# Kernel tuning notes

Measured on AMD Instinct MI355X. Metric: run time of the kernel, lower is better.

Reference implementation:

```python
import jax, jax.numpy as jnp
import numpy as np

B, L, D = 2, 2048, 2048
H, Hd = 16, 128


def _rotary_cos_sin(max_len, dim, base=10000.0):
    inv_freq = 1.0 / (base ** (np.arange(0, dim, 2, dtype=np.float32) / dim))
    t = np.arange(max_len, dtype=np.float32)
    freqs = np.outer(t, inv_freq)                      # [L, dim/2]
    emb = np.concatenate([freqs, freqs], axis=-1)      # [L, dim]
    cos = np.cos(emb)[None, None]                      # [1,1,L,dim]
    sin = np.sin(emb)[None, None]
    return jnp.asarray(cos), jnp.asarray(sin)


def setup_inputs() -> dict:
    key = jax.random.key(0)
    ks = jax.random.split(key, 5)
    hidden_states = jax.random.normal(ks[0], (B, L, D), dtype=jnp.float32)
    cos, sin = _rotary_cos_sin(L, Hd)
    s = 1.0 / np.sqrt(D)
    wq = jax.random.normal(ks[1], (H * Hd, D), dtype=jnp.float32) * s
    wk = jax.random.normal(ks[2], (H * Hd, D), dtype=jnp.float32) * s
    wv = jax.random.normal(ks[3], (H * Hd, D), dtype=jnp.float32) * s
    wo = jax.random.normal(ks[4], (D, H * Hd), dtype=jnp.float32) * s
    return {"hidden_states": hidden_states, "cos": cos, "sin": sin,
            "wq": wq, "wk": wk, "wv": wv, "wo": wo}


def _rotate_half(x):
    x1, x2 = jnp.split(x, 2, axis=-1)
    return jnp.concatenate([-x2, x1], axis=-1)


def reference(hidden_states, cos, sin, wq, wk, wv, wo):
    b, l, d = hidden_states.shape
    # QKV projections -> [B, H, L, Hd]
    q = (hidden_states @ wq.T).reshape(b, l, H, Hd).transpose(0, 2, 1, 3)
    k = (hidden_states @ wk.T).reshape(b, l, H, Hd).transpose(0, 2, 1, 3)
    v = (hidden_states @ wv.T).reshape(b, l, H, Hd).transpose(0, 2, 1, 3)
    c = cos[:, :, :l, :]
    s = sin[:, :, :l, :]
    q = q * c + _rotate_half(q) * s
    k = k * c + _rotate_half(k) * s
    # SDPA (non-causal, default scale = 1/sqrt(head_dim))
    scale = 1.0 / jnp.sqrt(jnp.asarray(Hd, dtype=q.dtype))
    scores = jnp.einsum('bhqd,bhkd->bhqk', q, k) * scale
    attn = jax.nn.softmax(scores, axis=-1)
    out = jnp.einsum('bhqk,bhkd->bhqd', attn, v)       # [B,H,L,Hd]
    out = out.transpose(0, 2, 1, 3).reshape(b, l, H * Hd)
    return out @ wo.T
```

## Files before the change

kernel.cpp:

```cpp
#include <hip/hip_runtime.h>

constexpr int Bb = 2;
constexpr int Ll = 2048;
constexpr int Dd = 2048;
constexpr int Hh = 16;
constexpr int Hd = 128;
constexpr int M  = Bb * Ll;

typedef __attribute__((ext_vector_type(8)))  short s16x8;
typedef __attribute__((ext_vector_type(4)))  float f32x4;
typedef __attribute__((ext_vector_type(16))) float f32x16;

__device__ __forceinline__ unsigned short f2bf(float f) {
    union { float f; unsigned u; } v; v.f = f;
    unsigned r = v.u + 0x7fffu + ((v.u >> 16) & 1u);
    return (unsigned short)(r >> 16);
}
__device__ __forceinline__ float bf2f(unsigned short b) {
    union { unsigned u; float f; } v; v.u = ((unsigned)b) << 16;
    return v.f;
}
__device__ __forceinline__ float fast_exp2(float x) {
#if __has_builtin(__builtin_amdgcn_exp2f)
    return __builtin_amdgcn_exp2f(x);
#else
    return exp2f(x);
#endif
}

__device__ __forceinline__ void gld16(const void* g, void* l) {
#if __has_builtin(__builtin_amdgcn_global_load_lds)
    __builtin_amdgcn_global_load_lds(
        (const __attribute__((address_space(1))) unsigned int*)g,
        (__attribute__((address_space(3))) unsigned int*)l, 16, 0, 0);
#else
    int lane = threadIdx.x & 63;
    ((int4*)l)[lane] = ((const int4*)g)[0];
#endif
}

__global__ __launch_bounds__(256)
void f2bf_all(const float* __restrict__ x,  const float* __restrict__ wq,
              const float* __restrict__ wk, const float* __restrict__ wv,
              const float* __restrict__ wo,
              unsigned short* __restrict__ Xb,  unsigned short* __restrict__ Wqb,
              unsigned short* __restrict__ Wkb, unsigned short* __restrict__ Wvb,
              unsigned short* __restrict__ Wob)
{
    int bid = blockIdx.x;
    const float* in; unsigned short* out; int off;
    if      (bid <  8192) { in = x;  out = Xb;  off = bid; }
    else if (bid < 12288) { in = wq; out = Wqb; off = bid - 8192; }
    else if (bid < 16384) { in = wk; out = Wkb; off = bid - 12288; }
    else if (bid < 20480) { in = wv; out = Wvb; off = bid - 16384; }
    else                  { in = wo; out = Wob; off = bid - 20480; }
    int i = (off * 256 + threadIdx.x) * 4;
    float4 v = *(const float4*)(in + i);
    ushort4 o;
    o.x = f2bf(v.x); o.y = f2bf(v.y); o.z = f2bf(v.z); o.w = f2bf(v.w);
    *(ushort4*)(out + i) = o;
}

__global__ __launch_bounds__(256, 2)
void mfma_gemm_qkv(const unsigned short* __restrict__ A,
                   const unsigned short* __restrict__ Wall,
                   unsigned short* __restrict__ Oq,
                   unsigned short* __restrict__ Ok,
                   unsigned short* __restrict__ Ov)
{
    constexpr int K  = 2048;
    constexpr int NT = K / 64;
    constexpr int BM = 128, BN = 192;
    constexpr int SLOT_US = (BM + BN) * 64;

    __shared__ unsigned short lds[2 * SLOT_US];

    const int t    = threadIdx.x;
    const int w    = t >> 6, lane = t & 63;
    const int wm   = w >> 1, wn = w & 1;
    const int m0   = blockIdx.y * BM, n0 = blockIdx.x * BN;
    const int r16  = lane & 15, q4 = lane >> 4;
    const int lxor = (r16 & 7) << 4;

    const int srow8 = lane >> 3;
    const int sgcol = (((lane & 7) ^ srow8) << 4);
    const char* Agb = (const char*)A;
    const char* Wgb = (const char*)Wall;

    f32x4 acc[4][6];
#pragma unroll
    for (int i = 0; i < 4; ++i)
#pragma unroll
        for (int j = 0; j < 6; ++j)
            acc[i][j] = (f32x4){0.f, 0.f, 0.f, 0.f};

#define STAGE_ALL(tt, sl) do {                                               \
    _Pragma("unroll") for (int p = 0; p < 4; ++p) {                          \
        int ia_ = w * 4 + p;                                                 \
        gld16(Agb + (size_t)(m0 + ia_ * 8 + srow8) * (K * 2) + (tt) * 128 + sgcol, \
              &lds[(sl) * SLOT_US + ia_ * 512]);                             \
    }                                                                        \
    _Pragma("unroll") for (int p = 0; p < 6; ++p) {                          \
        int ib_ = w * 6 + p;                                                 \
        gld16(Wgb + (size_t)(n0 + ib_ * 8 + srow8) * (K * 2) + (tt) * 128 + sgcol, \
              &lds[(sl) * SLOT_US + BM * 64 + ib_ * 512]);                   \
    }                                                                        \
} while (0)

#define MFMA24() do {                                                        \
    __builtin_amdgcn_s_setprio(1);                                           \
    _Pragma("unroll") for (int mi = 0; mi < 4; ++mi)                         \
    _Pragma("unroll") for (int ni = 0; ni < 6; ++ni)                         \
        acc[mi][ni] = __builtin_amdgcn_mfma_f32_16x16x32_bf16(                \
            a[mi], b[ni], acc[mi][ni], 0, 0, 0);                             \
    __builtin_amdgcn_s_setprio(0);                                           \
} while (0)

    STAGE_ALL(0, 0);
    asm volatile("s_waitcnt vmcnt(0)" ::: "memory");
    __builtin_amdgcn_s_barrier();
    asm volatile("" ::: "memory");

    for (int tt = 0; tt < NT; ++tt) {
        const int slot = tt & 1;
        const char* Ab = (const char*)&lds[slot * SLOT_US];
        const char* Bp = (const char*)&lds[slot * SLOT_US + BM * 64];
        const int c0 = (q4 * 16) ^ lxor;
        const int c1 = (64 + q4 * 16) ^ lxor;

        s16x8 a[4], b[6];

#pragma unroll
        for (int mi = 0; mi < 4; ++mi)
            a[mi] = *(const s16x8*)(Ab + (wm * 64 + mi * 16 + r16) * 128 + c0);
#pragma unroll
        for (int ni = 0; ni < 6; ++ni)
            b[ni] = *(const s16x8*)(Bp + (wn * 96 + ni * 16 + r16) * 128 + c0);
        if (tt + 1 < NT) STAGE_ALL(tt + 1, slot ^ 1);
        MFMA24();

#pragma unroll
        for (int mi = 0; mi < 4; ++mi)
            a[mi] = *(const s16x8*)(Ab + (wm * 64 + mi * 16 + r16) * 128 + c1);
#pragma unroll
        for (int ni = 0; ni < 6; ++ni)
            b[ni] = *(const s16x8*)(Bp + (wn * 96 + ni * 16 + r16) * 128 + c1);
        MFMA24();

        asm volatile("s_waitcnt vmcnt(0)" ::: "memory");
        __builtin_amdgcn_s_barrier();
        asm volatile("" ::: "memory");
    }
#undef STAGE_ALL
#undef MFMA24

#pragma unroll
    for (int ni = 0; ni < 6; ++ni) {
        int nb   = n0 + wn * 96 + ni * 16;
        int nsel = nb >> 11;
        int nr   = nb & 2047;
        int h    = nr >> 7;
        int d    = (nr & 127) + r16;
        if (nsel < 2) {
            unsigned short* O = nsel ? Ok : Oq;
#pragma unroll
            for (int mi = 0; mi < 4; ++mi)
#pragma unroll
                for (int r = 0; r < 4; ++r) {
                    int m = m0 + wm * 64 + mi * 16 + q4 * 4 + r;
                    int b = m >> 11, l = m & 2047;
                    O[(((size_t)b * Hh + h) * Ll + l) * Hd + d] =
                        f2bf(acc[mi][ni][r]);
                }
        } else {
#pragma unroll
            for (int mi = 0; mi < 4; ++mi) {
                int mb = m0 + wm * 64 + mi * 16 + q4 * 4;
                int b = mb >> 11, l = mb & 2047;
                ushort4 pk;
                pk.x = f2bf(acc[mi][ni][0]);
                pk.y = f2bf(acc[mi][ni][1]);
                pk.z = f2bf(acc[mi][ni][2]);
                pk.w = f2bf(acc[mi][ni][3]);
                *(ushort4*)&Ov[(((size_t)b * Hh + h) * Hd + d) * Ll + l] = pk;
            }
        }
    }
}

__global__ __launch_bounds__(256, 2)
void mfma_gemm_out(const unsigned short* __restrict__ A,
                   const unsigned short* __restrict__ W,
                   float* __restrict__ FO)
{
    constexpr int K  = 2048;
    constexpr int NT = K / 64;
    constexpr int BM = 128, BN = 128;
    constexpr int SLOT_US = (BM + BN) * 64;

    __shared__ unsigned short lds[2 * SLOT_US];

    const int t    = threadIdx.x;
    const int w    = t >> 6, lane = t & 63;
    const int wm   = w >> 1, wn = w & 1;
    const int m0   = blockIdx.y * BM, n0 = blockIdx.x * BN;
    const int r16  = lane & 15, q4 = lane >> 4;
    const int lxor = (r16 & 7) << 4;

    const int srow8 = lane >> 3;
    const int sgcol = (((lane & 7) ^ srow8) << 4);
    const char* Agb = (const char*)A;
    const char* Wgb = (const char*)W;

    f32x4 acc[4][4];
#pragma unroll
    for (int i = 0; i < 4; ++i)
#pragma unroll
        for (int j = 0; j < 4; ++j)
            acc[i][j] = (f32x4){0.f, 0.f, 0.f, 0.f};

#define STAGE_ALL(tt, sl) do {                                               \
    _Pragma("unroll") for (int p = 0; p < 4; ++p) {                          \
        int ia_ = w * 4 + p;                                                 \
        gld16(Agb + (size_t)(m0 + ia_ * 8 + srow8) * (K * 2) + (tt) * 128 + sgcol, \
              &lds[(sl) * SLOT_US + ia_ * 512]);                             \
    }                                                                        \
    _Pragma("unroll") for (int p = 0; p < 4; ++p) {                          \
        int ib_ = w * 4 + p;                                                 \
        gld16(Wgb + (size_t)(n0 + ib_ * 8 + srow8) * (K * 2) + (tt) * 128 + sgcol, \
              &lds[(sl) * SLOT_US + BM * 64 + ib_ * 512]);                   \
    }                                                                        \
} while (0)

#define MFMA16() do {                                                        \
    __builtin_amdgcn_s_setprio(1);                                           \
    _Pragma("unroll") for (int mi = 0; mi < 4; ++mi)                         \
    _Pragma("unroll") for (int ni = 0; ni < 4; ++ni)                         \
        acc[mi][ni] = __builtin_amdgcn_mfma_f32_16x16x32_bf16(                \
            a[mi], b[ni], acc[mi][ni], 0, 0, 0);                             \
    __builtin_amdgcn_s_setprio(0);                                           \
} while (0)

    STAGE_ALL(0, 0);
    asm volatile("s_waitcnt vmcnt(0)" ::: "memory");
    __builtin_amdgcn_s_barrier();
    asm volatile("" ::: "memory");

    for (int tt = 0; tt < NT; ++tt) {
        const int slot = tt & 1;
        const char* Ab = (const char*)&lds[slot * SLOT_US];
        const char* Bp = (const char*)&lds[slot * SLOT_US + BM * 64];
        const int c0 = (q4 * 16) ^ lxor;
        const int c1 = (64 + q4 * 16) ^ lxor;

        s16x8 a[4], b[4];

#pragma unroll
        for (int mi = 0; mi < 4; ++mi)
            a[mi] = *(const s16x8*)(Ab + (wm * 64 + mi * 16 + r16) * 128 + c0);
#pragma unroll
        for (int ni = 0; ni < 4; ++ni)
            b[ni] = *(const s16x8*)(Bp + (wn * 64 + ni * 16 + r16) * 128 + c0);
        if (tt + 1 < NT) STAGE_ALL(tt + 1, slot ^ 1);
        MFMA16();

#pragma unroll
        for (int mi = 0; mi < 4; ++mi)
            a[mi] = *(const s16x8*)(Ab + (wm * 64 + mi * 16 + r16) * 128 + c1);
#pragma unroll
        for (int ni = 0; ni < 4; ++ni)
            b[ni] = *(const s16x8*)(Bp + (wn * 64 + ni * 16 + r16) * 128 + c1);
        MFMA16();

        asm volatile("s_waitcnt vmcnt(0)" ::: "memory");
        __builtin_amdgcn_s_barrier();
        asm volatile("" ::: "memory");
    }
#undef STAGE_ALL
#undef MFMA16

#pragma unroll
    for (int mi = 0; mi < 4; ++mi)
#pragma unroll
        for (int ni = 0; ni < 4; ++ni) {
            int n = n0 + wn * 64 + ni * 16 + r16;
#pragma unroll
            for (int r = 0; r < 4; ++r) {
                int m = m0 + wm * 64 + mi * 16 + q4 * 4 + r;
                FO[(size_t)m * Dd + n] = acc[mi][ni][r];
            }
        }
}

__global__ __launch_bounds__(256)
void rope_bf16(unsigned short* __restrict__ q, unsigned short* __restrict__ k,
               const float* __restrict__ cosb, const float* __restrict__ sinb)
{
    const float QS = 0.1275175f;
    const int t = threadIdx.x;
    int rblk = blockIdx.x;
    unsigned short* base;
    float sc;
    if (rblk < 4096) { base = q; sc = QS; }
    else             { base = k; sc = 1.0f; rblk -= 4096; }

    const int row = rblk * 16 + (t >> 4);
    const int l   = row & (Ll - 1);
    const int d0  = (t & 15) * 8;
    unsigned short* xr = base + (size_t)row * Hd;

    s16x8 v0 = *(const s16x8*)(xr + d0);
    s16x8 vp = *(const s16x8*)(xr + (d0 ^ 64));
    const float* cp = cosb + (size_t)l * Hd + d0;
    const float* sp = sinb + (size_t)l * Hd + d0;
    float4 c0 = *(const float4*)cp,       c1 = *(const float4*)(cp + 4);
    float4 sa = *(const float4*)sp,       sb = *(const float4*)(sp + 4);
    const float cc[8] = {c0.x, c0.y, c0.z, c0.w, c1.x, c1.y, c1.z, c1.w};
    const float ss[8] = {sa.x, sa.y, sa.z, sa.w, sb.x, sb.y, sb.z, sb.w};
    const float sgn = (d0 < 64) ? -1.f : 1.f;

    s16x8 o;
#pragma unroll
    for (int j = 0; j < 8; ++j) {
        float a = bf2f((unsigned short)v0[j]);
        float p = bf2f((unsigned short)vp[j]);
        float res = fmaf(a, cc[j], sgn * p * ss[j]) * sc;
        o[j] = (short)f2bf(res);
    }
    asm volatile("" ::: "memory");
    *(s16x8*)(xr + d0) = o;
}

__global__ __launch_bounds__(256)
void flash_attn(const unsigned short* __restrict__ q,
                const unsigned short* __restrict__ k,
                const unsigned short* __restrict__ vT,
                unsigned short* __restrict__ ctx)
{
    __shared__ unsigned short Ks[2][64 * 128];
    __shared__ unsigned short Vs[2][128 * 64];
    __shared__ unsigned short Ps[4][32 * 64];

    const int t = threadIdx.x;
    const int w = t >> 6, lane = t & 63;
    const int n32 = lane & 31, half = lane >> 5;
    const int bh = blockIdx.x >> 4;
    const int l0 = (blockIdx.x & 15) * 128;

    const unsigned short* qb = q  + ((size_t)bh * Ll + l0 + w * 32) * Hd;
    const unsigned short* kb = k  + (size_t)bh * Ll * Hd;
    const unsigned short* vb = vT + (size_t)bh * Hd * Ll;

    const int k_r = lane >> 4, k_u = lane & 15;
    const int v_r = lane >> 3, v_u = lane & 7;

#define STAGE(J0, bsel) do {                                                  \
    _Pragma("unroll") for (int p = 0; p < 4; ++p) {                           \
        int j_ = w * 4 + p;                                                   \
        int row_ = j_ * 4 + k_r;                                              \
        gld16(kb + (size_t)((J0) + row_) * Hd + ((k_u ^ (row_ & 7)) * 8),     \
              &Ks[bsel][j_ * 512]);                                           \
    }                                                                         \
    _Pragma("unroll") for (int p = 0; p < 4; ++p) {                           \
        int j_ = w * 4 + p;                                                   \
        int row_ = j_ * 8 + v_r;                                              \
        gld16(vb + (size_t)row_ * Ll + (J0) + ((v_u ^ (row_ & 7)) * 8),       \
              &Vs[bsel][j_ * 512]);                                           \
    }                                                                         \
} while (0)

    s16x8 qf[8];
#pragma unroll
    for (int ks = 0; ks < 8; ++ks)
        qf[ks] = *(const s16x8*)(qb + (size_t)n32 * Hd + ks * 16 + half * 8);

    f32x16 o[4];
    float lacc[16];
#pragma unroll
    for (int nt = 0; nt < 4; ++nt)
#pragma unroll
        for (int r = 0; r < 16; ++r) o[nt][r] = 0.f;
#pragma unroll
    for (int r = 0; r < 16; ++r) lacc[r] = 0.f;

    unsigned short* Pw = Ps[w];
    const int psw = (n32 & 7) << 3;

    STAGE(0, 0);
    __syncthreads();

    int buf = 0;
    for (int j0 = 0; j0 < Ll; j0 += 64) {
        if (j0 + 64 < Ll) STAGE(j0 + 64, buf ^ 1);

        f32x16 s0, s1;
#pragma unroll
        for (int r = 0; r < 16; ++r) { s0[r] = 0.f; s1[r] = 0.f; }
        __builtin_amdgcn_s_setprio(1);
#pragma unroll
        for (int ks = 0; ks < 8; ++ks) {
            int kc = (ks * 16 + half * 8) ^ psw;
            s16x8 b0 = *(const s16x8*)&Ks[buf][n32 * 128 + kc];
            s16x8 b1 = *(const s16x8*)&Ks[buf][(32 + n32) * 128 + kc];
            s0 = __builtin_amdgcn_mfma_f32_32x32x16_bf16(qf[ks], b0, s0, 0, 0, 0);
            s1 = __builtin_amdgcn_mfma_f32_32x32x16_bf16(qf[ks], b1, s1, 0, 0, 0);
        }
        __builtin_amdgcn_s_setprio(0);

#pragma unroll
        for (int r = 0; r < 16; ++r) {
            int mrow = (r & 3) + 8 * (r >> 2) + 4 * half;
            int sw = (mrow & 7) << 3;
            float p0 = fast_exp2(s0[r]);
            float p1 = fast_exp2(s1[r]);
            lacc[r] += p0 + p1;
            union { float f; unsigned u; } u0, u1;
            u0.f = p0; u1.f = p1;
            Pw[mrow * 64 + (n32 ^ sw)]        = (unsigned short)((u0.u + 0x8000u) >> 16);
            Pw[mrow * 64 + ((32 + n32) ^ sw)] = (unsigned short)((u1.u + 0x8000u) >> 16);
        }

        __builtin_amdgcn_s_setprio(1);
#pragma unroll
        for (int kst = 0; kst < 4; ++kst) {
            int cc = (kst * 16 + half * 8) ^ psw;
            s16x8 pf2 = *(const s16x8*)&Pw[n32 * 64 + cc];
#pragma unroll
            for (int nt = 0; nt < 4; ++nt) {
                s16x8 vf = *(const s16x8*)&Vs[buf][(nt * 32 + n32) * 64 + cc];
                o[nt] = __builtin_amdgcn_mfma_f32_32x32x16_bf16(pf2, vf, o[nt], 0, 0, 0);
            }
        }
        __builtin_amdgcn_s_setprio(0);

        __syncthreads();
        buf ^= 1;
    }
#undef STAGE

    float linv[16];
#pragma unroll
    for (int r = 0; r < 16; ++r) {
        float s = lacc[r];
        s += __shfl_xor(s, 1, 64);
        s += __shfl_xor(s, 2, 64);
        s += __shfl_xor(s, 4, 64);
        s += __shfl_xor(s, 8, 64);
        s += __shfl_xor(s, 16, 64);
        linv[r] = 1.0f / s;
    }

    const int b = bh >> 4, h = bh & 15;
#pragma unroll
    for (int nt = 0; nt < 4; ++nt)
#pragma unroll
        for (int r = 0; r < 16; ++r) {
            int mrow = (r & 3) + 8 * (r >> 2) + 4 * half;
            int lq = l0 + w * 32 + mrow;
            ctx[((size_t)(b * Ll + lq)) * Dd + h * Hd + nt * 32 + n32] =
                f2bf(o[nt][r] * linv[r]);
        }
}

extern "C" void kernel_launch(void* const* d_in, const int* in_sizes, int n_in,
                              void* d_out, int out_size, void* d_ws, size_t ws_size,
                              hipStream_t stream)
{
    const float* hs   = (const float*)d_in[0];
    const float* cosb = (const float*)d_in[1];
    const float* sinb = (const float*)d_in[2];
    const float* wq   = (const float*)d_in[3];
    const float* wk   = (const float*)d_in[4];
    const float* wv   = (const float*)d_in[5];
    const float* wo   = (const float*)d_in[6];
    float* out = (float*)d_out;

    char* ws = (char*)d_ws;
    unsigned short* Xb  = (unsigned short*)(ws);
    unsigned short* Wqb = (unsigned short*)(ws + (16ull << 20));
    unsigned short* Wkb = (unsigned short*)(ws + (24ull << 20));
    unsigned short* Wvb = (unsigned short*)(ws + (32ull << 20));
    unsigned short* Wob = (unsigned short*)(ws + (40ull << 20));
    unsigned short* qb  = (unsigned short*)(ws + (48ull << 20));
    unsigned short* kb  = (unsigned short*)(ws + (64ull << 20));
    unsigned short* vTb = (unsigned short*)(ws + (80ull << 20));
    unsigned short* ctx = Xb;

    f2bf_all<<<dim3(24576), dim3(256), 0, stream>>>(
        hs, wq, wk, wv, wo, Xb, Wqb, Wkb, Wvb, Wob);

    mfma_gemm_qkv<<<dim3(6144 / 192, M / 128), dim3(256), 0, stream>>>(
        Xb, Wqb, qb, kb, vTb);

    rope_bf16<<<dim3(2 * (Bb * Hh * Ll) / 16), dim3(256), 0, stream>>>(
        qb, kb, cosb, sinb);

    flash_attn<<<dim3(Bb * Hh * (Ll / 128)), dim3(256), 0, stream>>>(qb, kb, vTb, ctx);

    mfma_gemm_out<<<dim3(Dd / 128, M / 128), dim3(256), 0, stream>>>(
        ctx, Wob, out);
}
```

Measured before the change: 379.6 us.

## Fuse RoPE and Q scaling into QKV GEMM epilogue via LDS staging

Removes the separate rope_bf16 kernel by applying rotary embedding and the query scale inside the QKV GEMM epilogue. The GEMM N-tile shrinks from 192 to 128 columns so each block covers exactly one head of q, k or v. Accumulators are staged as fp32 in padded LDS so each thread can read both rotate-half partners. This saves a launch plus a bf16 read/write pass over q and k, and rounds to bf16 only once. The cost is a smaller tile with lower reuse, a larger grid, and an extra LDS round trip and barrier in the epilogue.

```diff
diff --git a/kernel.cpp b/kernel.cpp
--- a/kernel.cpp
+++ b/kernel.cpp
@@ -64,21 +64,27 @@
 __global__ __launch_bounds__(256, 2)
 void mfma_gemm_qkv(const unsigned short* __restrict__ A,
                    const unsigned short* __restrict__ Wall,
+                   const float* __restrict__ cosb,
+                   const float* __restrict__ sinb,
                    unsigned short* __restrict__ Oq,
                    unsigned short* __restrict__ Ok,
                    unsigned short* __restrict__ Ov)
 {
     constexpr int K  = 2048;
     constexpr int NT = K / 64;
-    constexpr int BM = 128, BN = 192;
+    constexpr int BM = 128, BN = 128;
     constexpr int SLOT_US = (BM + BN) * 64;
 
-    __shared__ unsigned short lds[2 * SLOT_US];
+    __shared__ float ldsf[128 * 132];
+    unsigned short* lds = (unsigned short*)ldsf;
 
     const int t    = threadIdx.x;
     const int w    = t >> 6, lane = t & 63;
     const int wm   = w >> 1, wn = w & 1;
-    const int m0   = blockIdx.y * BM, n0 = blockIdx.x * BN;
+    const int bx   = blockIdx.x;
+    const int nsel = bx >> 4;
+    const int h    = bx & 15;
+    const int m0   = blockIdx.y * BM, n0 = bx * BN;
     const int r16  = lane & 15, q4 = lane >> 4;
     const int lxor = (r16 & 7) << 4;
 
@@ -86,131 +92,6 @@
     const int sgcol = (((lane & 7) ^ srow8) << 4);
     const char* Agb = (const char*)A;
     const char* Wgb = (const char*)Wall;
-
-    f32x4 acc[4][6];
-#pragma unroll
-    for (int i = 0; i < 4; ++i)
-#pragma unroll
-        for (int j = 0; j < 6; ++j)
-            acc[i][j] = (f32x4){0.f, 0.f, 0.f, 0.f};
-
-#define STAGE_ALL(tt, sl) do {                                               \
-    _Pragma("unroll") for (int p = 0; p < 4; ++p) {                          \
-        int ia_ = w * 4 + p;                                                 \
-        gld16(Agb + (size_t)(m0 + ia_ * 8 + srow8) * (K * 2) + (tt) * 128 + sgcol, \
-              &lds[(sl) * SLOT_US + ia_ * 512]);                             \
-    }                                                                        \
-    _Pragma("unroll") for (int p = 0; p < 6; ++p) {                          \
-        int ib_ = w * 6 + p;                                                 \
-        gld16(Wgb + (size_t)(n0 + ib_ * 8 + srow8) * (K * 2) + (tt) * 128 + sgcol, \
-              &lds[(sl) * SLOT_US + BM * 64 + ib_ * 512]);                   \
-    }                                                                        \
-} while (0)
-
-#define MFMA24() do {                                                        \
-    __builtin_amdgcn_s_setprio(1);                                           \
-    _Pragma("unroll") for (int mi = 0; mi < 4; ++mi)                         \
-    _Pragma("unroll") for (int ni = 0; ni < 6; ++ni)                         \
-        acc[mi][ni] = __builtin_amdgcn_mfma_f32_16x16x32_bf16(                \
-            a[mi], b[ni], acc[mi][ni], 0, 0, 0);                             \
-    __builtin_amdgcn_s_setprio(0);                                           \
-} while (0)
-
-    STAGE_ALL(0, 0);
-    asm volatile("s_waitcnt vmcnt(0)" ::: "memory");
-    __builtin_amdgcn_s_barrier();
-    asm volatile("" ::: "memory");
-
-    for (int tt = 0; tt < NT; ++tt) {
-        const int slot = tt & 1;
-        const char* Ab = (const char*)&lds[slot * SLOT_US];
-        const char* Bp = (const char*)&lds[slot * SLOT_US + BM * 64];
-        const int c0 = (q4 * 16) ^ lxor;
-        const int c1 = (64 + q4 * 16) ^ lxor;
-
-        s16x8 a[4], b[6];
-
-#pragma unroll
-        for (int mi = 0; mi < 4; ++mi)
-            a[mi] = *(const s16x8*)(Ab + (wm * 64 + mi * 16 + r16) * 128 + c0);
-#pragma unroll
-        for (int ni = 0; ni < 6; ++ni)
-            b[ni] = *(const s16x8*)(Bp + (wn * 96 + ni * 16 + r16) * 128 + c0);
-        if (tt + 1 < NT) STAGE_ALL(tt + 1, slot ^ 1);
-        MFMA24();
-
-#pragma unroll
-        for (int mi = 0; mi < 4; ++mi)
-            a[mi] = *(const s16x8*)(Ab + (wm * 64 + mi * 16 + r16) * 128 + c1);
-#pragma unroll
-        for (int ni = 0; ni < 6; ++ni)
-            b[ni] = *(const s16x8*)(Bp + (wn * 96 + ni * 16 + r16) * 128 + c1);
-        MFMA24();
-
-        asm volatile("s_waitcnt vmcnt(0)" ::: "memory");
-        __builtin_amdgcn_s_barrier();
-        asm volatile("" ::: "memory");
-    }
-#undef STAGE_ALL
-#undef MFMA24
-
-#pragma unroll
-    for (int ni = 0; ni < 6; ++ni) {
-        int nb   = n0 + wn * 96 + ni * 16;
-        int nsel = nb >> 11;
-        int nr   = nb & 2047;
-        int h    = nr >> 7;
-        int d    = (nr & 127) + r16;
-        if (nsel < 2) {
-            unsigned short* O = nsel ? Ok : Oq;
-#pragma unroll
-            for (int mi = 0; mi < 4; ++mi)
-#pragma unroll
-                for (int r = 0; r < 4; ++r) {
-                    int m = m0 + wm * 64 + mi * 16 + q4 * 4 + r;
-                    int b = m >> 11, l = m & 2047;
-                    O[(((size_t)b * Hh + h) * Ll + l) * Hd + d] =
-                        f2bf(acc[mi][ni][r]);
-                }
-        } else {
-#pragma unroll
-            for (int mi = 0; mi < 4; ++mi) {
-                int mb = m0 + wm * 64 + mi * 16 + q4 * 4;
-                int b = mb >> 11, l = mb & 2047;
-                ushort4 pk;
-                pk.x = f2bf(acc[mi][ni][0]);
-                pk.y = f2bf(acc[mi][ni][1]);
-                pk.z = f2bf(acc[mi][ni][2]);
-                pk.w = f2bf(acc[mi][ni][3]);
-                *(ushort4*)&Ov[(((size_t)b * Hh + h) * Hd + d) * Ll + l] = pk;
-            }
-        }
-    }
-}
-
-__global__ __launch_bounds__(256, 2)
-void mfma_gemm_out(const unsigned short* __restrict__ A,
-                   const unsigned short* __restrict__ W,
-                   float* __restrict__ FO)
-{
-    constexpr int K  = 2048;
-    constexpr int NT = K / 64;
-    constexpr int BM = 128, BN = 128;
-    constexpr int SLOT_US = (BM + BN) * 64;
-
-    __shared__ unsigned short lds[2 * SLOT_US];
-
-    const int t    = threadIdx.x;
-    const int w    = t >> 6, lane = t & 63;
-    const int wm   = w >> 1, wn = w & 1;
-    const int m0   = blockIdx.y * BM, n0 = blockIdx.x * BN;
-    const int r16  = lane & 15, q4 = lane >> 4;
-    const int lxor = (r16 & 7) << 4;
-
-    const int srow8 = lane >> 3;
-    const int sgcol = (((lane & 7) ^ srow8) << 4);
-    const char* Agb = (const char*)A;
-    const char* Wgb = (const char*)W;
 
     f32x4 acc[4][4];
 #pragma unroll
@@ -279,6 +160,156 @@
 #undef STAGE_ALL
 #undef MFMA16
 
+    if (nsel == 2) {
+#pragma unroll
+        for (int mi = 0; mi < 4; ++mi) {
+            int mb = m0 + wm * 64 + mi * 16 + q4 * 4;
+            int b = mb >> 11, l = mb & 2047;
+#pragma unroll
+            for (int ni = 0; ni < 4; ++ni) {
+                int d = wn * 64 + ni * 16 + r16;
+                ushort4 pk;
+                pk.x = f2bf(acc[mi][ni][0]);
+                pk.y = f2bf(acc[mi][ni][1]);
+                pk.z = f2bf(acc[mi][ni][2]);
+                pk.w = f2bf(acc[mi][ni][3]);
+                *(ushort4*)&Ov[(((size_t)b * Hh + h) * Hd + d) * Ll + l] = pk;
+            }
+        }
+    } else {
+#pragma unroll
+        for (int mi = 0; mi < 4; ++mi)
+#pragma unroll
+            for (int ni = 0; ni < 4; ++ni) {
+                int col = wn * 64 + ni * 16 + r16;
+#pragma unroll
+                for (int r = 0; r < 4; ++r) {
+                    int row = wm * 64 + mi * 16 + q4 * 4 + r;
+                    ldsf[row * 132 + col] = acc[mi][ni][r];
+                }
+            }
+        __syncthreads();
+
+        const float sc  = (nsel == 0) ? 0.1275175f : 1.0f;
+        unsigned short* O = (nsel == 0) ? Oq : Ok;
+        const int row = t >> 1;
+        const int d0  = (t & 1) * 64;
+        const float sgn = (t & 1) ? 1.f : -1.f;
+        const int m = m0 + row, b = m >> 11, l = m & 2047;
+        const float* Lr = ldsf + row * 132;
+        const float* cp = cosb + (size_t)l * Hd + d0;
+        const float* sp = sinb + (size_t)l * Hd + d0;
+        unsigned short* Orow = O + (((size_t)b * Hh + h) * Ll + l) * Hd + d0;
+#pragma unroll
+        for (int j = 0; j < 64; j += 4) {
+            float4 c4 = *(const float4*)(cp + j);
+            float4 s4 = *(const float4*)(sp + j);
+            float x0, xp;
+            ushort4 pk;
+            x0 = Lr[d0 + j + 0]; xp = Lr[(d0 ^ 64) + j + 0];
+            pk.x = f2bf(fmaf(x0, c4.x, sgn * xp * s4.x) * sc);
+            x0 = Lr[d0 + j + 1]; xp = Lr[(d0 ^ 64) + j + 1];
+            pk.y = f2bf(fmaf(x0, c4.y, sgn * xp * s4.y) * sc);
+            x0 = Lr[d0 + j + 2]; xp = Lr[(d0 ^ 64) + j + 2];
+            pk.z = f2bf(fmaf(x0, c4.z, sgn * xp * s4.z) * sc);
+            x0 = Lr[d0 + j + 3]; xp = Lr[(d0 ^ 64) + j + 3];
+            pk.w = f2bf(fmaf(x0, c4.w, sgn * xp * s4.w) * sc);
+            *(ushort4*)(Orow + j) = pk;
+        }
+    }
+}
+
+__global__ __launch_bounds__(256, 2)
+void mfma_gemm_out(const unsigned short* __restrict__ A,
+                   const unsigned short* __restrict__ W,
+                   float* __restrict__ FO)
+{
+    constexpr int K  = 2048;
+    constexpr int NT = K / 64;
+    constexpr int BM = 128, BN = 128;
+    constexpr int SLOT_US = (BM + BN) * 64;
+
+    __shared__ unsigned short lds[2 * SLOT_US];
+
+    const int t    = threadIdx.x;
+    const int w    = t >> 6, lane = t & 63;
+    const int wm   = w >> 1, wn = w & 1;
+    const int m0   = blockIdx.y * BM, n0 = blockIdx.x * BN;
+    const int r16  = lane & 15, q4 = lane >> 4;
+    const int lxor = (r16 & 7) << 4;
+
+    const int srow8 = lane >> 3;
+    const int sgcol = (((lane & 7) ^ srow8) << 4);
+    const char* Agb = (const char*)A;
+    const char* Wgb = (const char*)W;
+
+    f32x4 acc[4][4];
+#pragma unroll
+    for (int i = 0; i < 4; ++i)
+#pragma unroll
+        for (int j = 0; j < 4; ++j)
+            acc[i][j] = (f32x4){0.f, 0.f, 0.f, 0.f};
+
+#define STAGE_ALL(tt, sl) do {                                               \
+    _Pragma("unroll") for (int p = 0; p < 4; ++p) {                          \
+        int ia_ = w * 4 + p;                                                 \
+        gld16(Agb + (size_t)(m0 + ia_ * 8 + srow8) * (K * 2) + (tt) * 128 + sgcol, \
+              &lds[(sl) * SLOT_US + ia_ * 512]);                             \
+    }                                                                        \
+    _Pragma("unroll") for (int p = 0; p < 4; ++p) {                          \
+        int ib_ = w * 4 + p;                                                 \
+        gld16(Wgb + (size_t)(n0 + ib_ * 8 + srow8) * (K * 2) + (tt) * 128 + sgcol, \
+              &lds[(sl) * SLOT_US + BM * 64 + ib_ * 512]);                   \
+    }                                                                        \
+} while (0)
+
+#define MFMA16() do {                                                        \
+    __builtin_amdgcn_s_setprio(1);                                           \
+    _Pragma("unroll") for (int mi = 0; mi < 4; ++mi)                         \
+    _Pragma("unroll") for (int ni = 0; ni < 4; ++ni)                         \
+        acc[mi][ni] = __builtin_amdgcn_mfma_f32_16x16x32_bf16(                \
+            a[mi], b[ni], acc[mi][ni], 0, 0, 0);                             \
+    __builtin_amdgcn_s_setprio(0);                                           \
+} while (0)
+
+    STAGE_ALL(0, 0);
+    asm volatile("s_waitcnt vmcnt(0)" ::: "memory");
+    __builtin_amdgcn_s_barrier();
+    asm volatile("" ::: "memory");
+
+    for (int tt = 0; tt < NT; ++tt) {
+        const int slot = tt & 1;
+        const char* Ab = (const char*)&lds[slot * SLOT_US];
+        const char* Bp = (const char*)&lds[slot * SLOT_US + BM * 64];
+        const int c0 = (q4 * 16) ^ lxor;
+        const int c1 = (64 + q4 * 16) ^ lxor;
+
+        s16x8 a[4], b[4];
+
+#pragma unroll
+        for (int mi = 0; mi < 4; ++mi)
+            a[mi] = *(const s16x8*)(Ab + (wm * 64 + mi * 16 + r16) * 128 + c0);
+#pragma unroll
+        for (int ni = 0; ni < 4; ++ni)
+            b[ni] = *(const s16x8*)(Bp + (wn * 64 + ni * 16 + r16) * 128 + c0);
+        if (tt + 1 < NT) STAGE_ALL(tt + 1, slot ^ 1);
+        MFMA16();
+
+#pragma unroll
+        for (int mi = 0; mi < 4; ++mi)
+            a[mi] = *(const s16x8*)(Ab + (wm * 64 + mi * 16 + r16) * 128 + c1);
+#pragma unroll
+        for (int ni = 0; ni < 4; ++ni)
+            b[ni] = *(const s16x8*)(Bp + (wn * 64 + ni * 16 + r16) * 128 + c1);
+        MFMA16();
+
+        asm volatile("s_waitcnt vmcnt(0)" ::: "memory");
+        __builtin_amdgcn_s_barrier();
+        asm volatile("" ::: "memory");
+    }
+#undef STAGE_ALL
+#undef MFMA16
+
 #pragma unroll
     for (int mi = 0; mi < 4; ++mi)
 #pragma unroll
@@ -290,45 +321,6 @@
                 FO[(size_t)m * Dd + n] = acc[mi][ni][r];
             }
         }
-}
-
-__global__ __launch_bounds__(256)
-void rope_bf16(unsigned short* __restrict__ q, unsigned short* __restrict__ k,
-               const float* __restrict__ cosb, const float* __restrict__ sinb)
-{
-    const float QS = 0.1275175f;
-    const int t = threadIdx.x;
-    int rblk = blockIdx.x;
-    unsigned short* base;
-    float sc;
-    if (rblk < 4096) { base = q; sc = QS; }
-    else             { base = k; sc = 1.0f; rblk -= 4096; }
-
-    const int row = rblk * 16 + (t >> 4);
-    const int l   = row & (Ll - 1);
-    const int d0  = (t & 15) * 8;
-    unsigned short* xr = base + (size_t)row * Hd;
-
-    s16x8 v0 = *(const s16x8*)(xr + d0);
-    s16x8 vp = *(const s16x8*)(xr + (d0 ^ 64));
-    const float* cp = cosb + (size_t)l * Hd + d0;
-    const float* sp = sinb + (size_t)l * Hd + d0;
-    float4 c0 = *(const float4*)cp,       c1 = *(const float4*)(cp + 4);
-    float4 sa = *(const float4*)sp,       sb = *(const float4*)(sp + 4);
-    const float cc[8] = {c0.x, c0.y, c0.z, c0.w, c1.x, c1.y, c1.z, c1.w};
-    const float ss[8] = {sa.x, sa.y, sa.z, sa.w, sb.x, sb.y, sb.z, sb.w};
-    const float sgn = (d0 < 64) ? -1.f : 1.f;
-
-    s16x8 o;
-#pragma unroll
-    for (int j = 0; j < 8; ++j) {
-        float a = bf2f((unsigned short)v0[j]);
-        float p = bf2f((unsigned short)vp[j]);
-        float res = fmaf(a, cc[j], sgn * p * ss[j]) * sc;
-        o[j] = (short)f2bf(res);
-    }
-    asm volatile("" ::: "memory");
-    *(s16x8*)(xr + d0) = o;
 }
 
 __global__ __launch_bounds__(256)
@@ -489,11 +481,8 @@
     f2bf_all<<<dim3(24576), dim3(256), 0, stream>>>(
         hs, wq, wk, wv, wo, Xb, Wqb, Wkb, Wvb, Wob);
 
-    mfma_gemm_qkv<<<dim3(6144 / 192, M / 128), dim3(256), 0, stream>>>(
-        Xb, Wqb, qb, kb, vTb);
-
-    rope_bf16<<<dim3(2 * (Bb * Hh * Ll) / 16), dim3(256), 0, stream>>>(
-        qb, kb, cosb, sinb);
+    mfma_gemm_qkv<<<dim3(6144 / 128, M / 128), dim3(256), 0, stream>>>(
+        Xb, Wqb, cosb, sinb, qb, kb, vTb);
 
     flash_attn<<<dim3(Bb * Hh * (Ll / 128)), dim3(256), 0, stream>>>(qb, kb, vTb, ctx);
 
```

New measurement: 391.5 us. 3.1% more time.

## Fuse RoPE into QKV GEMM epilogue via permuted Q/K weight rows

Applied to the files above, without the earlier changes.

Permutes the Q and K weight rows during bf16 conversion so that each rotary pair (d, d+64) sits in adjacent output columns. The QKV GEMM epilogue can then apply RoPE and the query scale with a lane shuffle plus cos/sin loads. This removes the separate rope kernel launch and its extra read/write pass over Q and K. In exchange the epilogue gets scattered cos/sin loads and a less coalesced store pattern.

```diff
diff --git a/kernel.cpp b/kernel.cpp
--- a/kernel.cpp
+++ b/kernel.cpp
@@ -48,22 +48,31 @@
               unsigned short* __restrict__ Wob)
 {
     int bid = blockIdx.x;
-    const float* in; unsigned short* out; int off;
+    const float* in; unsigned short* out; int off; bool perm = false;
     if      (bid <  8192) { in = x;  out = Xb;  off = bid; }
-    else if (bid < 12288) { in = wq; out = Wqb; off = bid - 8192; }
-    else if (bid < 16384) { in = wk; out = Wkb; off = bid - 12288; }
+    else if (bid < 12288) { in = wq; out = Wqb; off = bid - 8192;  perm = true; }
+    else if (bid < 16384) { in = wk; out = Wkb; off = bid - 12288; perm = true; }
     else if (bid < 20480) { in = wv; out = Wvb; off = bid - 16384; }
     else                  { in = wo; out = Wob; off = bid - 20480; }
     int i = (off * 256 + threadIdx.x) * 4;
+    size_t j = (size_t)i;
+    if (perm) {
+        int n = i >> 11;
+        int c = i & 2047;
+        int p = (n & ~127) | (((n & 63) << 1) | ((n >> 6) & 1));
+        j = ((size_t)p << 11) | c;
+    }
     float4 v = *(const float4*)(in + i);
     ushort4 o;
     o.x = f2bf(v.x); o.y = f2bf(v.y); o.z = f2bf(v.z); o.w = f2bf(v.w);
-    *(ushort4*)(out + i) = o;
+    *(ushort4*)(out + j) = o;
 }
 
 __global__ __launch_bounds__(256, 2)
 void mfma_gemm_qkv(const unsigned short* __restrict__ A,
                    const unsigned short* __restrict__ Wall,
+                   const float* __restrict__ cosb,
+                   const float* __restrict__ sinb,
                    unsigned short* __restrict__ Oq,
                    unsigned short* __restrict__ Ok,
                    unsigned short* __restrict__ Ov)
@@ -160,19 +169,28 @@
         int nsel = nb >> 11;
         int nr   = nb & 2047;
         int h    = nr >> 7;
-        int d    = (nr & 127) + r16;
         if (nsel < 2) {
+            const float sc = (nsel == 0) ? 0.1275175f : 1.0f;
             unsigned short* O = nsel ? Ok : Oq;
+            int p127 = (nr & 127) + r16;
+            int dd   = p127 >> 1;
+            int d    = ((p127 & 1) << 6) | dd;
+            float sgn = (p127 & 1) ? 1.f : -1.f;
 #pragma unroll
             for (int mi = 0; mi < 4; ++mi)
 #pragma unroll
                 for (int r = 0; r < 4; ++r) {
                     int m = m0 + wm * 64 + mi * 16 + q4 * 4 + r;
                     int b = m >> 11, l = m & 2047;
-                    O[(((size_t)b * Hh + h) * Ll + l) * Hd + d] =
-                        f2bf(acc[mi][ni][r]);
+                    float x  = acc[mi][ni][r];
+                    float xp = __shfl_xor(x, 1, 64);
+                    float c  = cosb[(size_t)l * Hd + dd];
+                    float s  = sinb[(size_t)l * Hd + dd];
+                    float res = fmaf(x, c, sgn * xp * s) * sc;
+                    O[(((size_t)b * Hh + h) * Ll + l) * Hd + d] = f2bf(res);
                 }
         } else {
+            int d = (nr & 127) + r16;
 #pragma unroll
             for (int mi = 0; mi < 4; ++mi) {
                 int mb = m0 + wm * 64 + mi * 16 + q4 * 4;
@@ -290,45 +308,6 @@
                 FO[(size_t)m * Dd + n] = acc[mi][ni][r];
             }
         }
-}
-
-__global__ __launch_bounds__(256)
-void rope_bf16(unsigned short* __restrict__ q, unsigned short* __restrict__ k,
-               const float* __restrict__ cosb, const float* __restrict__ sinb)
-{
-    const float QS = 0.1275175f;
-    const int t = threadIdx.x;
-    int rblk = blockIdx.x;
-    unsigned short* base;
-    float sc;
-    if (rblk < 4096) { base = q; sc = QS; }
-    else             { base = k; sc = 1.0f; rblk -= 4096; }
-
-    const int row = rblk * 16 + (t >> 4);
-    const int l   = row & (Ll - 1);
-    const int d0  = (t & 15) * 8;
-    unsigned short* xr = base + (size_t)row * Hd;
-
-    s16x8 v0 = *(const s16x8*)(xr + d0);
-    s16x8 vp = *(const s16x8*)(xr + (d0 ^ 64));
-    const float* cp = cosb + (size_t)l * Hd + d0;
-    const float* sp = sinb + (size_t)l * Hd + d0;
-    float4 c0 = *(const float4*)cp,       c1 = *(const float4*)(cp + 4);
-    float4 sa = *(const float4*)sp,       sb = *(const float4*)(sp + 4);
-    const float cc[8] = {c0.x, c0.y, c0.z, c0.w, c1.x, c1.y, c1.z, c1.w};
-    const float ss[8] = {sa.x, sa.y, sa.z, sa.w, sb.x, sb.y, sb.z, sb.w};
-    const float sgn = (d0 < 64) ? -1.f : 1.f;
-
-    s16x8 o;
-#pragma unroll
-    for (int j = 0; j < 8; ++j) {
-        float a = bf2f((unsigned short)v0[j]);
-        float p = bf2f((unsigned short)vp[j]);
-        float res = fmaf(a, cc[j], sgn * p * ss[j]) * sc;
-        o[j] = (short)f2bf(res);
-    }
-    asm volatile("" ::: "memory");
-    *(s16x8*)(xr + d0) = o;
 }
 
 __global__ __launch_bounds__(256)
@@ -490,10 +469,7 @@
         hs, wq, wk, wv, wo, Xb, Wqb, Wkb, Wvb, Wob);
 
     mfma_gemm_qkv<<<dim3(6144 / 192, M / 128), dim3(256), 0, stream>>>(
-        Xb, Wqb, qb, kb, vTb);
-
-    rope_bf16<<<dim3(2 * (Bb * Hh * Ll) / 16), dim3(256), 0, stream>>>(
-        qb, kb, cosb, sinb);
+        Xb, Wqb, cosb, sinb, qb, kb, vTb);
 
     flash_attn<<<dim3(Bb * Hh * (Ll / 128)), dim3(256), 0, stream>>>(qb, kb, vTb, ctx);
 
```

After: 370.1 us. -2.5%, faster.
